# Kernel optimization log

Measured on AMD Instinct MI355X. Metric: run time of the kernel, lower is better.

## Reference

```python
import jax, jax.numpy as jnp
import numpy as np

N = 4096          # nodes (= Mamba sequence length)
E_EDGES = 65536   # edges
D = 512           # dim_h (= d_inner, expand=1)
NEXP = 4          # num_experts (cfg.model.num_experts)
DSTATE = 16
DCONV = 4
DTRANK = 32       # ceil(D/16)
EPS = 1e-5


def _silu(x):
    return x * jax.nn.sigmoid(x)


def _bn(h, g, b):
    # BatchNorm1d over node axis (batch statistics)
    mu = h.mean(0)
    var = h.var(0)
    return (h - mu) * jax.lax.rsqrt(var + EPS) * g + b


def _mamba(u, in_w, conv_w, conv_b, x_w, dt_w, dt_b, A_log, Dp, out_w):
    # u: [L, D] single-sequence Mamba(d_model=D, d_state=16, d_conv=4, expand=1)
    L = u.shape[0]
    xz = u @ in_w                      # [L, 2D]
    xc, z = xz[:, :D], xz[:, D:]
    xp = jnp.pad(xc, ((DCONV - 1, 0), (0, 0)))
    xconv = conv_b
    for k in range(DCONV):             # depthwise causal conv, tiny fixed loop
        xconv = xconv + conv_w[:, k] * xp[k:k + L]
    xs = _silu(xconv)                  # [L, D]
    dbc = xs @ x_w                     # [L, DTRANK + 2*DSTATE]
    dt = jax.nn.softplus(dbc[:, :DTRANK] @ dt_w + dt_b)          # [L, D]
    Bm = dbc[:, DTRANK:DTRANK + DSTATE]                          # [L, S]
    Cm = dbc[:, DTRANK + DSTATE:]                                # [L, S]
    A = -jnp.exp(A_log)                                          # [D, S]
    dA = jnp.exp(dt[:, :, None] * A[None])                       # [L, D, S]
    dBu = dt[:, :, None] * Bm[:, None, :] * xs[:, :, None]       # [L, D, S]

    def step(hprev, inp):
        dA_t, dBu_t, C_t = inp
        hn = dA_t * hprev + dBu_t
        return hn, (hn * C_t[None, :]).sum(-1)

    _, ys = jax.lax.scan(step, jnp.zeros((D, DSTATE), u.dtype), (dA, dBu, Cm))
    y = ys + Dp * xs
    return (y * _silu(z)) @ out_w      # [L, D]


def setup_inputs() -> dict:
    key = jax.random.key(0)
    ks = jax.random.split(key, 24)
    s = 1.0 / np.sqrt(D)
    inp = {}
    inp['x'] = jax.random.normal(ks[0], (N, D), jnp.float32)
    inp['edge_index'] = jax.random.randint(ks[1], (2, E_EDGES), 0, N)
    inp['edge_attr'] = jax.random.normal(ks[2], (E_EDGES, D), jnp.float32)
    # GINE nn: Linear(D,D) -> ReLU -> Linear(D,D)
    inp['gin_w1'] = jax.random.normal(ks[3], (D, D)) * s
    inp['gin_b1'] = jnp.zeros((D,))
    inp['gin_w2'] = jax.random.normal(ks[4], (D, D)) * s
    inp['gin_b2'] = jnp.zeros((D,))
    # BatchNorms
    inp['bn1l_g'] = jnp.ones((D,)); inp['bn1l_b'] = jnp.zeros((D,))
    inp['bn1a_g'] = jnp.ones((D,)); inp['bn1a_b'] = jnp.zeros((D,))
    inp['bn2_g'] = jnp.ones((D,)); inp['bn2_b'] = jnp.zeros((D,))
    # gating MLP [D, D//2, NEXP]
    inp['gate_w1'] = jax.random.normal(ks[5], (D, D // 2)) * s
    inp['gate_b1'] = jnp.zeros((D // 2,))
    inp['gate_w2'] = jax.random.normal(ks[6], (D // 2, NEXP)) * (1.0 / np.sqrt(D // 2))
    inp['gate_b2'] = jnp.zeros((NEXP,))
    # stacked per-expert Mamba params
    inp['in_w'] = jax.random.normal(ks[7], (NEXP, D, 2 * D)) * s
    inp['conv_w'] = jax.random.normal(ks[8], (NEXP, D, DCONV)) * 0.5
    inp['conv_b'] = jnp.zeros((NEXP, D))
    inp['x_w'] = jax.random.normal(ks[9], (NEXP, D, DTRANK + 2 * DSTATE)) * s
    inp['dt_w'] = jax.random.normal(ks[10], (NEXP, DTRANK, D)) * (1.0 / np.sqrt(DTRANK))
    inp['dt_b'] = jax.random.normal(ks[11], (NEXP, D)) * 0.1 - 4.0
    A0 = jnp.log(jnp.arange(1, DSTATE + 1, dtype=jnp.float32))
    inp['A_log'] = jnp.broadcast_to(A0, (NEXP, D, DSTATE)).copy()
    inp['Dp'] = jnp.ones((NEXP, D))
    inp['out_w'] = jax.random.normal(ks[12], (NEXP, D, D)) * s
    # FFN
    inp['ff_w1'] = jax.random.normal(ks[13], (D, 2 * D)) * s
    inp['ff_b1'] = jnp.zeros((2 * D,))
    inp['ff_w2'] = jax.random.normal(ks[14], (2 * D, D)) * (1.0 / np.sqrt(2 * D))
    inp['ff_b2'] = jnp.zeros((D,))
    return inp


def reference(x, edge_index, edge_attr,
              gin_w1, gin_b1, gin_w2, gin_b2,
              bn1l_g, bn1l_b, bn1a_g, bn1a_b, bn2_g, bn2_b,
              gate_w1, gate_b1, gate_w2, gate_b2,
              in_w, conv_w, conv_b, x_w, dt_w, dt_b, A_log, Dp, out_w,
              ff_w1, ff_b1, ff_w2, ff_b2):
    h_in = x
    src, dst = edge_index[0], edge_index[1]
    # local GINEConv: nn(x + sum_j relu(x_j + e_ji))
    msg = jax.nn.relu(x[src] + edge_attr)                      # [E, D]
    aggr = jax.ops.segment_sum(msg, dst, num_segments=N)       # [N, D]
    h_local = jax.nn.relu((x + aggr) @ gin_w1 + gin_b1) @ gin_w2 + gin_b2
    h_local = _bn(h_in + h_local, bn1l_g, bn1l_b)
    # gated mixture of Mamba experts
    gate = jax.nn.softmax(jax.nn.relu(x @ gate_w1 + gate_b1) @ gate_w2 + gate_b2, axis=-1)  # [N, NEXP]
    ys = jax.vmap(_mamba, in_axes=(None, 0, 0, 0, 0, 0, 0, 0, 0, 0))(
        x, in_w, conv_w, conv_b, x_w, dt_w, dt_b, A_log, Dp, out_w)  # [NEXP, N, D]
    h_attn = jnp.einsum('ne,end->nd', gate, ys)
    h_attn = _bn(h_in + h_attn, bn1a_g, bn1a_b)
    # fuse + FFN
    h = h_local + h_attn
    ff = jax.nn.relu(h @ ff_w1 + ff_b1) @ ff_w2 + ff_b2
    return _bn(h + ff, bn2_g, bn2_b)
```

## Files before the change

kernel.cpp:

```cpp
#include <hip/hip_runtime.h>
#include <hip/hip_bf16.h>
#include <math.h>

#define N_NODES 4096
#define E_EDGE 65536
#define D 512
#define NEXP 4
#define DSTATE 16
#define DCONV 4
#define DTRANK 32
#define EPS 1e-5f
#define LCHUNK 32
#define NCHUNK (N_NODES / LCHUNK)

typedef __hip_bfloat16 bf16;
typedef short bf16x8 __attribute__((ext_vector_type(8)));
typedef float f32x4 __attribute__((ext_vector_type(4)));
typedef unsigned short u16x4 __attribute__((ext_vector_type(4)));

__device__ __forceinline__ float siluf(float x) { return x / (1.f + __expf(-x)); }
__device__ __forceinline__ float softplusf(float x) {
  return (x > 20.f) ? x : log1pf(__expf(x));
}
__device__ __forceinline__ unsigned short f2bf(float v) {
  bf16 b = __float2bfloat16(v);
  return *reinterpret_cast<unsigned short*>(&b);
}

__device__ __forceinline__ void gload16(const void* g, void* l) {
  __builtin_amdgcn_global_load_lds(
      (const __attribute__((address_space(1))) void*)g,
      (__attribute__((address_space(3))) void*)l, 16, 0, 0);
}

template <int FN, int EPI>
__global__ __launch_bounds__(256, 2) void mm_k(
    const bf16* __restrict__ A, int lda, long sA,
    const bf16* __restrict__ Bt, int ldb, long sB,
    const float* __restrict__ bias,
    float* __restrict__ Cf, bf16* __restrict__ Cb, int ldc, long sC, int K) {
  constexpr int BN = FN * 32;
  __shared__ __align__(16) bf16 As[128 * 32];
  __shared__ __align__(16) bf16 Bs[BN * 32];
  const int z = blockIdx.z;
  A += (size_t)z * sA;
  Bt += (size_t)z * sB;
  const int tid = threadIdx.x;
  const int w = tid >> 6, l = tid & 63;
  const int wr = w >> 1, wc = w & 1;
  const int bm = blockIdx.y * 128, bn = blockIdx.x * BN;

  f32x4 acc[4][FN];
#pragma unroll
  for (int i = 0; i < 4; ++i)
#pragma unroll
    for (int j = 0; j < FN; ++j) acc[i][j] = 0.f;

  const int srow = l >> 2, schunk = l & 3;
  const bf16* gA = A + (size_t)(bm + w * 16 + srow) * lda + schunk * 8;
  const bf16* gB = Bt + (size_t)(bn + w * 16 + srow) * ldb + schunk * 8;
  bf16* lA = As + w * 512;
  bf16* lB = Bs + w * 512;

  const int ar = wr * 64 + (l & 15);
  const int br = wc * FN * 16 + (l & 15);
  const int kb = l >> 4;

  for (int k0 = 0; k0 < K; k0 += 32) {
    gload16(gA + k0, lA);
    gload16(gA + k0 + (size_t)64 * lda, lA + 64 * 32);
    gload16(gB + k0, lB);
    if (FN == 4) gload16(gB + k0 + (size_t)64 * ldb, lB + 64 * 32);
    __syncthreads();
    const bf16x8* Ap = (const bf16x8*)As;
    const bf16x8* Bp = (const bf16x8*)Bs;
    bf16x8 af[4], bfr[FN];
#pragma unroll
    for (int i = 0; i < 4; ++i) af[i] = Ap[(ar + i * 16) * 4 + kb];
#pragma unroll
    for (int j = 0; j < FN; ++j) bfr[j] = Bp[(br + j * 16) * 4 + kb];
#pragma unroll
    for (int i = 0; i < 4; ++i)
#pragma unroll
      for (int j = 0; j < FN; ++j)
        acc[i][j] = __builtin_amdgcn_mfma_f32_16x16x32_bf16(bfr[j], af[i], acc[i][j], 0, 0, 0);
    __syncthreads();
  }

  if (Cf) Cf += (size_t)z * sC;
  if (Cb) Cb += (size_t)z * sC;
  const int r0 = bm + wr * 64 + (l & 15);
  const int cb0 = bn + wc * FN * 16 + ((l >> 4) << 2);
#pragma unroll
  for (int i = 0; i < 4; ++i) {
    const int row = r0 + i * 16;
#pragma unroll
    for (int j = 0; j < FN; ++j) {
      const int col = cb0 + j * 16;
      f32x4 v = acc[i][j];
      if (bias) v += *(const f32x4*)&bias[col];
      if (EPI == 1) {
#pragma unroll
        for (int r = 0; r < 4; ++r) v[r] = fmaxf(v[r], 0.f);
      }
      if (Cf) *(f32x4*)&Cf[(size_t)row * ldc + col] = v;
      if (Cb) {
        u16x4 u;
#pragma unroll
        for (int r = 0; r < 4; ++r) u[r] = f2bf(v[r]);
        *(u16x4*)&Cb[(size_t)row * ldc + col] = u;
      }
    }
  }
}

struct WtArgs {
  const float* in[8];
  bf16* out[8];
  int K[8], N[8], ldo[8];
  long sin[8], sout[8];
  int cum[8];
};
__global__ __launch_bounds__(256) void wtrans_all_k(WtArgs a) {
  __shared__ float t[32][33];
  int b = blockIdx.x;
  int i = 0;
  while (b >= a.cum[i]) ++i;
  int local = b - (i ? a.cum[i - 1] : 0);
  const int ntx = a.N[i] / 32;
  const int nty = a.K[i] / 32;
  const int perz = ntx * nty;
  const int z = local / perz;
  const int rem = local - z * perz;
  const int bx = rem % ntx, by = rem / ntx;
  const float* in = a.in[i] + (size_t)z * a.sin[i];
  bf16* out = a.out[i] + (size_t)z * a.sout[i];
  const int N = a.N[i], ldo = a.ldo[i];
  const int n0 = bx * 32, k0 = by * 32;
  const int tx = threadIdx.x & 31, ty = threadIdx.x >> 5;
  for (int r = ty; r < 32; r += 8) t[r][tx] = in[(size_t)(k0 + r) * N + n0 + tx];
  __syncthreads();
  for (int r = ty; r < 32; r += 8)
    out[(size_t)(n0 + r) * ldo + k0 + tx] = __float2bfloat16(t[tx][r]);
}

__global__ void hist_k(const int* __restrict__ ei, int* __restrict__ deg) {
  int e = blockIdx.x * 256 + threadIdx.x;
  if (e < E_EDGE) atomicAdd(&deg[ei[E_EDGE + e]], 1);
}

__global__ __launch_bounds__(1024) void prefix_k(const int* __restrict__ deg,
                                                 int* __restrict__ rowstart) {
  __shared__ int s[1024];
  int t = threadIdx.x;
  int base = t * 4;
  int d0 = deg[base], d1 = deg[base + 1], d2 = deg[base + 2], d3 = deg[base + 3];
  int sum = d0 + d1 + d2 + d3;
  s[t] = sum;
  __syncthreads();
  for (int off = 1; off < 1024; off <<= 1) {
    int v = (t >= off) ? s[t - off] : 0;
    __syncthreads();
    s[t] += v;
    __syncthreads();
  }
  int excl = s[t] - sum;
  rowstart[base] = excl;
  rowstart[base + 1] = excl + d0;
  rowstart[base + 2] = excl + d0 + d1;
  rowstart[base + 3] = excl + d0 + d1 + d2;
}

__global__ void scatter_k(const int* __restrict__ ei, const int* __restrict__ rowstart,
                          int* __restrict__ cnt, int* __restrict__ eid) {
  int e = blockIdx.x * 256 + threadIdx.x;
  if (e < E_EDGE) {
    int dst = ei[E_EDGE + e];
    int slot = rowstart[dst] + atomicAdd(&cnt[dst], 1);
    eid[slot] = e;
  }
}

__global__ __launch_bounds__(256) void aggr_gather_k(
    const float* __restrict__ x, const int* __restrict__ ei, const float* __restrict__ ea,
    const int* __restrict__ rowstart, const int* __restrict__ deg,
    const int* __restrict__ eid, bf16* __restrict__ hpre, bf16* __restrict__ xbf) {
  int n = blockIdx.x;
  int tid = threadIdx.x;
  int beg = rowstart[n];
  int end = beg + deg[n];
  float a0 = 0.f, a1 = 0.f;
  int i = beg;
  for (; i + 1 < end; i += 2) {
    int e0 = eid[i], e1 = eid[i + 1];
    int s0 = ei[e0], s1 = ei[e1];
    const float* x0 = x + (size_t)s0 * D;
    const float* e0p = ea + (size_t)e0 * D;
    const float* x1 = x + (size_t)s1 * D;
    const float* e1p = ea + (size_t)e1 * D;
    a0 += fmaxf(x0[tid] + e0p[tid], 0.f) + fmaxf(x1[tid] + e1p[tid], 0.f);
    a1 += fmaxf(x0[tid + 256] + e0p[tid + 256], 0.f) +
          fmaxf(x1[tid + 256] + e1p[tid + 256], 0.f);
  }
  if (i < end) {
    int e0 = eid[i];
    int s0 = ei[e0];
    const float* x0 = x + (size_t)s0 * D;
    const float* e0p = ea + (size_t)e0 * D;
    a0 += fmaxf(x0[tid] + e0p[tid], 0.f);
    a1 += fmaxf(x0[tid + 256] + e0p[tid + 256], 0.f);
  }
  float xv0 = x[(size_t)n * D + tid];
  float xv1 = x[(size_t)n * D + tid + 256];
  hpre[(size_t)n * D + tid] = __float2bfloat16(xv0 + a0);
  hpre[(size_t)n * D + tid + 256] = __float2bfloat16(xv1 + a1);
  xbf[(size_t)n * D + tid] = __float2bfloat16(xv0);
  xbf[(size_t)n * D + tid + 256] = __float2bfloat16(xv1);
}

__global__ __launch_bounds__(256) void gate2_k(const float* __restrict__ g1,
                                               const float* __restrict__ w2,
                                               const float* __restrict__ b2,
                                               float* __restrict__ gate) {
  int row = blockIdx.x * 4 + (threadIdx.x >> 6);
  int lane = threadIdx.x & 63;
  float a0 = 0.f, a1 = 0.f, a2 = 0.f, a3 = 0.f;
  for (int k = lane; k < 256; k += 64) {
    float v = g1[(size_t)row * 256 + k];
    a0 = fmaf(v, w2[k * 4 + 0], a0);
    a1 = fmaf(v, w2[k * 4 + 1], a1);
    a2 = fmaf(v, w2[k * 4 + 2], a2);
    a3 = fmaf(v, w2[k * 4 + 3], a3);
  }
#pragma unroll
  for (int off = 32; off; off >>= 1) {
    a0 += __shfl_down(a0, off);
    a1 += __shfl_down(a1, off);
    a2 += __shfl_down(a2, off);
    a3 += __shfl_down(a3, off);
  }
  if (lane == 0) {
    float l0 = a0 + b2[0], l1 = a1 + b2[1], l2 = a2 + b2[2], l3 = a3 + b2[3];
    float m = fmaxf(fmaxf(l0, l1), fmaxf(l2, l3));
    float e0 = __expf(l0 - m), e1 = __expf(l1 - m), e2 = __expf(l2 - m), e3 = __expf(l3 - m);
    float s = 1.f / (e0 + e1 + e2 + e3);
    gate[row * 4 + 0] = e0 * s;
    gate[row * 4 + 1] = e1 * s;
    gate[row * 4 + 2] = e2 * s;
    gate[row * 4 + 3] = e3 * s;
  }
}

__global__ void conv_silu_k(const bf16* __restrict__ xz, const float* __restrict__ cw,
                            const float* __restrict__ cb, bf16* __restrict__ xs, int e0) {
  const int z = blockIdx.y;
  xz += (size_t)z * N_NODES * 2 * D;
  xs += (size_t)z * N_NODES * D;
  cw += (size_t)(e0 + z) * D * DCONV;
  cb += (size_t)(e0 + z) * D;
  int idx = blockIdx.x * blockDim.x + threadIdx.x;
  if (idx >= N_NODES * D) return;
  int t = idx >> 9;
  int d = idx & (D - 1);
  float acc = cb[d];
#pragma unroll
  for (int k = 0; k < DCONV; ++k) {
    int tt = t + k - (DCONV - 1);
    if (tt >= 0)
      acc = fmaf(cw[d * DCONV + k], __bfloat162float(xz[(size_t)tt * (2 * D) + d]), acc);
  }
  xs[idx] = __float2bfloat16(siluf(acc));
}

__global__ void dt_k(const float* __restrict__ dbc, const float* __restrict__ dtw,
                     const float* __restrict__ dtbias, bf16* __restrict__ dt, int e0) {
  const int z = blockIdx.y;
  dbc += (size_t)z * N_NODES * 64;
  dt += (size_t)z * N_NODES * D;
  dtw += (size_t)(e0 + z) * DTRANK * D;
  dtbias += (size_t)(e0 + z) * D;
  int idx = blockIdx.x * blockDim.x + threadIdx.x;
  int t = idx >> 9, d = idx & (D - 1);
  float acc = dtbias[d];
#pragma unroll
  for (int k = 0; k < DTRANK; ++k) acc = fmaf(dbc[t * 64 + k], dtw[k * D + d], acc);
  dt[idx] = __float2bfloat16(softplusf(acc));
}

__global__ __launch_bounds__(256) void colstats_k(const float* __restrict__ p,
                                                  const float* __restrict__ q,
                                                  float* __restrict__ acc) {
  __shared__ float sb[4][512], sb2[4][512];
  const int w = threadIdx.x >> 6, l = threadIdx.x & 63;
  float s[8], s2[8];
#pragma unroll
  for (int i = 0; i < 8; ++i) { s[i] = 0.f; s2[i] = 0.f; }
  for (int j = 0; j < 16; ++j) {
    size_t base = ((size_t)blockIdx.x * 64 + w * 16 + j) * D;
#pragma unroll
    for (int i = 0; i < 8; ++i) {
      int c = i * 64 + l;
      float v = p[base + c] + q[base + c];
      s[i] += v;
      s2[i] = fmaf(v, v, s2[i]);
    }
  }
#pragma unroll
  for (int i = 0; i < 8; ++i) {
    sb[w][i * 64 + l] = s[i];
    sb2[w][i * 64 + l] = s2[i];
  }
  __syncthreads();
  for (int c = threadIdx.x; c < 512; c += 256) {
    atomicAdd(&acc[c], sb[0][c] + sb[1][c] + sb[2][c] + sb[3][c]);
    atomicAdd(&acc[512 + c], sb2[0][c] + sb2[1][c] + sb2[2][c] + sb2[3][c]);
  }
}

__global__ __launch_bounds__(256) void colstats2_k(const float* __restrict__ x,
                                                   const float* __restrict__ p,
                                                   const float* __restrict__ q,
                                                   float* __restrict__ acc1,
                                                   float* __restrict__ acc2) {
  __shared__ float sb[4][512], sb2[4][512];
  const int w = threadIdx.x >> 6, l = threadIdx.x & 63;
  float s1[8], s1q[8], s2[8], s2q[8];
#pragma unroll
  for (int i = 0; i < 8; ++i) { s1[i] = 0.f; s1q[i] = 0.f; s2[i] = 0.f; s2q[i] = 0.f; }
  for (int j = 0; j < 16; ++j) {
    size_t base = ((size_t)blockIdx.x * 64 + w * 16 + j) * D;
#pragma unroll
    for (int i = 0; i < 8; ++i) {
      int c = i * 64 + l;
      float xv = x[base + c];
      float v1 = xv + p[base + c];
      float v2 = xv + q[base + c];
      s1[i] += v1;
      s1q[i] = fmaf(v1, v1, s1q[i]);
      s2[i] += v2;
      s2q[i] = fmaf(v2, v2, s2q[i]);
    }
  }
#pragma unroll
  for (int i = 0; i < 8; ++i) {
    sb[w][i * 64 + l] = s1[i];
    sb2[w][i * 64 + l] = s1q[i];
  }
  __syncthreads();
  for (int c = threadIdx.x; c < 512; c += 256) {
    atomicAdd(&acc1[c], sb[0][c] + sb[1][c] + sb[2][c] + sb[3][c]);
    atomicAdd(&acc1[512 + c], sb2[0][c] + sb2[1][c] + sb2[2][c] + sb2[3][c]);
  }
  __syncthreads();
#pragma unroll
  for (int i = 0; i < 8; ++i) {
    sb[w][i * 64 + l] = s2[i];
    sb2[w][i * 64 + l] = s2q[i];
  }
  __syncthreads();
  for (int c = threadIdx.x; c < 512; c += 256) {
    atomicAdd(&acc2[c], sb[0][c] + sb[1][c] + sb[2][c] + sb[3][c]);
    atomicAdd(&acc2[512 + c], sb2[0][c] + sb2[1][c] + sb2[2][c] + sb2[3][c]);
  }
}

__device__ __forceinline__ void bn_params(const float* acc, int d, float& mu, float& rsig) {
  mu = acc[d] * (1.f / N_NODES);
  float var = acc[512 + d] * (1.f / N_NODES) - mu * mu;
  rsig = rsqrtf(var + EPS);
}

__global__ void norm_k(const float* __restrict__ p, const float* __restrict__ q,
                       const float* __restrict__ acc, const float* __restrict__ g,
                       const float* __restrict__ b, float* __restrict__ o) {
  int idx = blockIdx.x * blockDim.x + threadIdx.x;
  if (idx >= N_NODES * D) return;
  int d = idx & (D - 1);
  float mu, rsig;
  bn_params(acc, d, mu, rsig);
  o[idx] = (p[idx] + q[idx] - mu) * rsig * g[d] + b[d];
}

__global__ void bnadd2_k(const float* __restrict__ x, const float* __restrict__ hloc,
                         const float* __restrict__ hattn, const float* __restrict__ acc1,
                         const float* __restrict__ acc2, const float* __restrict__ g1,
                         const float* __restrict__ b1, const float* __restrict__ g2,
                         const float* __restrict__ b2, float* __restrict__ of,
                         bf16* __restrict__ ob) {
  int idx = blockIdx.x * blockDim.x + threadIdx.x;
  if (idx >= N_NODES * D) return;
  int d = idx & (D - 1);
  float mu1, rs1, mu2, rs2;
  bn_params(acc1, d, mu1, rs1);
  bn_params(acc2, d, mu2, rs2);
  float xv = x[idx];
  float v = (xv + hloc[idx] - mu1) * rs1 * g1[d] + b1[d] +
            (xv + hattn[idx] - mu2) * rs2 * g2[d] + b2[d];
  of[idx] = v;
  ob[idx] = __float2bfloat16(v);
}

__global__ __launch_bounds__(512) void scanA_k(const bf16* __restrict__ dt,
                                               const bf16* __restrict__ xs,
                                               const float* __restrict__ dbc,
                                               const float* __restrict__ Alog,
                                               float* __restrict__ Q,
                                               float* __restrict__ dtsum, int e0) {
  const int z = blockIdx.y;
  dt += (size_t)z * N_NODES * D;
  xs += (size_t)z * N_NODES * D;
  dbc += (size_t)z * N_NODES * 64;
  Alog += (size_t)(e0 + z) * D * DSTATE;
  Q += (size_t)z * NCHUNK * D * DSTATE;
  dtsum += (size_t)z * NCHUNK * D;
  int c = blockIdx.x;
  int d = threadIdx.x;
  float As[DSTATE], h[DSTATE];
#pragma unroll
  for (int s = 0; s < DSTATE; ++s) {
    As[s] = -__expf(Alog[d * DSTATE + s]);
    h[s] = 0.f;
  }
  float dts = 0.f;
  int t0 = c * LCHUNK;
  for (int t = t0; t < t0 + LCHUNK; ++t) {
    float dtv = __bfloat162float(dt[(size_t)t * D + d]);
    float xv = __bfloat162float(xs[(size_t)t * D + d]);
    float bx = dtv * xv;
    dts += dtv;
#pragma unroll
    for (int s = 0; s < DSTATE; ++s) {
      float Bv = dbc[(size_t)t * 64 + DTRANK + s];
      h[s] = fmaf(__expf(dtv * As[s]), h[s], bx * Bv);
    }
  }
  size_t base = ((size_t)c * D + d) * DSTATE;
#pragma unroll
  for (int s = 0; s < DSTATE; ++s) Q[base + s] = h[s];
  dtsum[c * D + d] = dts;
}

__global__ __launch_bounds__(256) void scanB_k(const float* __restrict__ Q,
                                               const float* __restrict__ dtsum,
                                               const float* __restrict__ Alog,
                                               float* __restrict__ Hin, int e0) {
  const int z = blockIdx.y;
  Q += (size_t)z * NCHUNK * D * DSTATE;
  dtsum += (size_t)z * NCHUNK * D;
  Alog += (size_t)(e0 + z) * D * DSTATE;
  Hin += (size_t)z * NCHUNK * D * DSTATE;
  int idx = blockIdx.x * blockDim.x + threadIdx.x;
  int d = idx >> 4;
  float As = -__expf(Alog[idx]);
  float h = 0.f;
  for (int c = 0; c < NCHUNK; ++c) {
    size_t base = (size_t)c * D * DSTATE + idx;
    Hin[base] = h;
    h = fmaf(__expf(As * dtsum[c * D + d]), h, Q[base]);
  }
}

__global__ __launch_bounds__(512) void scanC_k(const bf16* __restrict__ dt,
                                               const bf16* __restrict__ xs,
                                               const float* __restrict__ dbc,
                                               const float* __restrict__ Alog,
                                               const float* __restrict__ Hin,
                                               const bf16* __restrict__ xz,
                                               const float* __restrict__ Dp,
                                               const float* __restrict__ gate,
                                               bf16* __restrict__ u, int e0) {
  const int z = blockIdx.y;
  dt += (size_t)z * N_NODES * D;
  xs += (size_t)z * N_NODES * D;
  dbc += (size_t)z * N_NODES * 64;
  Alog += (size_t)(e0 + z) * D * DSTATE;
  Hin += (size_t)z * NCHUNK * D * DSTATE;
  xz += (size_t)z * N_NODES * 2 * D;
  Dp += (size_t)(e0 + z) * D;
  u += (size_t)(e0 + z) * 512;
  const int ge = e0 + z;
  int c = blockIdx.x;
  int d = threadIdx.x;
  float As[DSTATE], h[DSTATE];
  size_t base = ((size_t)c * D + d) * DSTATE;
#pragma unroll
  for (int s = 0; s < DSTATE; ++s) {
    As[s] = -__expf(Alog[d * DSTATE + s]);
    h[s] = Hin[base + s];
  }
  float Dv = Dp[d];
  int t0 = c * LCHUNK;
  for (int t = t0; t < t0 + LCHUNK; ++t) {
    float dtv = __bfloat162float(dt[(size_t)t * D + d]);
    float xv = __bfloat162float(xs[(size_t)t * D + d]);
    float bx = dtv * xv;
    float y = 0.f;
#pragma unroll
    for (int s = 0; s < DSTATE; ++s) {
      float Bv = dbc[(size_t)t * 64 + DTRANK + s];
      float Cv = dbc[(size_t)t * 64 + DTRANK + DSTATE + s];
      h[s] = fmaf(__expf(dtv * As[s]), h[s], bx * Bv);
      y = fmaf(h[s], Cv, y);
    }
    float zv = __bfloat162float(xz[(size_t)t * (2 * D) + D + d]);
    float gv = gate[t * NEXP + ge];
    u[(size_t)t * 2048 + d] = __float2bfloat16(gv * (y + Dv * xv) * siluf(zv));
  }
}

extern "C" void kernel_launch(void* const* d_in, const int* in_sizes, int n_in,
                              void* d_out, int out_size, void* d_ws, size_t ws_size,
                              hipStream_t stream) {
  const float* x = (const float*)d_in[0];
  const int* ei = (const int*)d_in[1];
  const float* ea = (const float*)d_in[2];
  const float* gin_w1 = (const float*)d_in[3];
  const float* gin_b1 = (const float*)d_in[4];
  const float* gin_w2 = (const float*)d_in[5];
  const float* gin_b2 = (const float*)d_in[6];
  const float* bn1l_g = (const float*)d_in[7];
  const float* bn1l_b = (const float*)d_in[8];
  const float* bn1a_g = (const float*)d_in[9];
  const float* bn1a_b = (const float*)d_in[10];
  const float* bn2_g = (const float*)d_in[11];
  const float* bn2_b = (const float*)d_in[12];
  const float* gate_w1 = (const float*)d_in[13];
  const float* gate_b1 = (const float*)d_in[14];
  const float* gate_w2 = (const float*)d_in[15];
  const float* gate_b2 = (const float*)d_in[16];
  const float* in_w = (const float*)d_in[17];
  const float* conv_w = (const float*)d_in[18];
  const float* conv_b = (const float*)d_in[19];
  const float* x_w = (const float*)d_in[20];
  const float* dt_w = (const float*)d_in[21];
  const float* dt_b = (const float*)d_in[22];
  const float* A_log = (const float*)d_in[23];
  const float* Dp = (const float*)d_in[24];
  const float* out_w = (const float*)d_in[25];
  const float* ff_w1 = (const float*)d_in[26];
  const float* ff_b1 = (const float*)d_in[27];
  const float* ff_w2 = (const float*)d_in[28];
  const float* ff_b2 = (const float*)d_in[29];
  float* out = (float*)d_out;

  const size_t ND = (size_t)N_NODES * D;
  const size_t NDb = ND / 2;

  const size_t fixed_f = 3 * ND + (size_t)N_NODES * 256 + 16384 + 2490624 + ND + 2048 +
                         81920 + 2 * ND + 4096;
  const size_t per_f = 2 * ND + NDb + (size_t)N_NODES * 64 + NDb +
                       2 * (size_t)NCHUNK * D * DSTATE + (size_t)NCHUNK * D;
  const int EB = (ws_size >= (fixed_f + 4 * per_f + 65536) * sizeof(float)) ? 4 : 1;

  float* ws = (float*)d_ws;
  size_t off = 0;
  auto alloc = [&](size_t n) {
    float* p = ws + off;
    off += (n + 63) & ~(size_t)63;
    return p;
  };
  float* ffo = alloc(ND);
  float* pbuf = alloc(ND);
  float* hlocal = alloc(ND);
  float* g1 = alloc((size_t)N_NODES * 256);
  float* gate = alloc((size_t)N_NODES * NEXP);
  bf16* gw1t = (bf16*)alloc(131072);
  bf16* gw2t = (bf16*)alloc(131072);
  bf16* gatew1t = (bf16*)alloc(65536);
  bf16* inwt = (bf16*)alloc(1048576);
  bf16* xwt = (bf16*)alloc(65536);
  bf16* outwt_cat = (bf16*)alloc(524288);
  bf16* ffw1t = (bf16*)alloc(262144);
  bf16* ffw2t = (bf16*)alloc(262144);
  int* deg = (int*)alloc(N_NODES);
  int* cnt = (int*)alloc(N_NODES);
  float* accs = alloc(3072);
  int* eid = (int*)alloc(E_EDGE);
  int* rowstart = (int*)alloc(N_NODES);
  float* xbf_f = alloc(NDb);
  float* xz_f = alloc((size_t)EB * ND);
  float* xs_f = alloc((size_t)EB * NDb);
  float* dbc = alloc((size_t)EB * N_NODES * 64);
  float* dtb_f = alloc((size_t)EB * NDb);
  float* Qb = alloc((size_t)EB * NCHUNK * D * DSTATE);
  float* Hin = alloc((size_t)EB * NCHUNK * D * DSTATE);
  float* dtsum = alloc((size_t)EB * NCHUNK * D);
  float* ucat_f = alloc(4 * NDb);
  float* hattn_raw = alloc(ND);
  float* acc1 = accs, *acc2 = accs + 1024, *acc3 = accs + 2048;

  bf16* x_bf = (bf16*)xbf_f;
  bf16* hpre_bf = (bf16*)pbuf;
  bf16* t1_bf = (bf16*)(pbuf + NDb);
  bf16* xz_bf = (bf16*)xz_f;
  bf16* xs_bf = (bf16*)xs_f;
  bf16* dt_bf = (bf16*)dtb_f;
  bf16* ucat = (bf16*)ucat_f;
  float* hcomb = xz_f;
  bf16* hcomb_bf = (bf16*)(ucat_f);
  bf16* ffh_bf = (bf16*)pbuf;

  const int nelem = N_NODES * D;
  const int ew = (nelem + 255) / 256;

  hipMemsetAsync(deg, 0, (N_NODES + N_NODES + 3072) * sizeof(float), stream);

  WtArgs wa;
  const float* wsrc[8] = {gin_w1, gin_w2, gate_w1, in_w, x_w, out_w, ff_w1, ff_w2};
  bf16* wdst[8] = {gw1t, gw2t, gatew1t, inwt, xwt, outwt_cat, ffw1t, ffw2t};
  int wK[8] = {512, 512, 512, 512, 512, 512, 512, 1024};
  int wN[8] = {512, 512, 256, 1024, 64, 512, 1024, 512};
  int wldo[8] = {512, 512, 512, 512, 512, 2048, 512, 1024};
  long wsin[8] = {0, 0, 0, (long)512 * 1024, (long)512 * 64, (long)512 * 512, 0, 0};
  long wsout[8] = {0, 0, 0, (long)512 * 1024, (long)64 * 512, 512, 0, 0};
  int wz[8] = {1, 1, 1, 4, 4, 4, 1, 1};
  int cum = 0;
  for (int i = 0; i < 8; ++i) {
    wa.in[i] = wsrc[i];
    wa.out[i] = wdst[i];
    wa.K[i] = wK[i];
    wa.N[i] = wN[i];
    wa.ldo[i] = wldo[i];
    wa.sin[i] = wsin[i];
    wa.sout[i] = wsout[i];
    cum += (wN[i] / 32) * (wK[i] / 32) * wz[i];
    wa.cum[i] = cum;
  }
  wtrans_all_k<<<cum, 256, 0, stream>>>(wa);

  hist_k<<<E_EDGE / 256, 256, 0, stream>>>(ei, deg);
  prefix_k<<<1, 1024, 0, stream>>>(deg, rowstart);
  scatter_k<<<E_EDGE / 256, 256, 0, stream>>>(ei, rowstart, cnt, eid);
  aggr_gather_k<<<N_NODES, 256, 0, stream>>>(x, ei, ea, rowstart, deg, eid, hpre_bf, x_bf);
  mm_k<2, 1><<<dim3(8, 32, 1), 256, 0, stream>>>(hpre_bf, 512, 0, gw1t, 512, 0, gin_b1,
                                                 nullptr, t1_bf, 512, 0, 512);
  mm_k<2, 0><<<dim3(8, 32, 1), 256, 0, stream>>>(t1_bf, 512, 0, gw2t, 512, 0, gin_b2,
                                                 hlocal, nullptr, 512, 0, 512);

  mm_k<2, 1><<<dim3(4, 32, 1), 256, 0, stream>>>(x_bf, 512, 0, gatew1t, 512, 0, gate_b1,
                                                 g1, nullptr, 256, 0, 512);
  gate2_k<<<N_NODES / 4, 256, 0, stream>>>(g1, gate_w2, gate_b2, gate);

  for (int e0 = 0; e0 < NEXP; e0 += EB) {
    mm_k<4, 0><<<dim3(8, 32, EB), 256, 0, stream>>>(
        x_bf, 512, 0, inwt + (size_t)e0 * 512 * 1024, 512, (long)512 * 1024, nullptr,
        nullptr, xz_bf, 1024, (long)N_NODES * 1024, 512);
    conv_silu_k<<<dim3(ew, EB), 256, 0, stream>>>(xz_bf, conv_w, conv_b, xs_bf, e0);
    mm_k<2, 0><<<dim3(1, 32, EB), 256, 0, stream>>>(
        xs_bf, 512, (long)ND, xwt + (size_t)e0 * 64 * 512, 512, (long)64 * 512, nullptr,
        dbc, nullptr, 64, (long)N_NODES * 64, 512);
    dt_k<<<dim3(ew, EB), 256, 0, stream>>>(dbc, dt_w, dt_b, dt_bf, e0);
    scanA_k<<<dim3(NCHUNK, EB), 512, 0, stream>>>(dt_bf, xs_bf, dbc, A_log, Qb, dtsum, e0);
    scanB_k<<<dim3((D * DSTATE) / 256, EB), 256, 0, stream>>>(Qb, dtsum, A_log, Hin, e0);
    scanC_k<<<dim3(NCHUNK, EB), 512, 0, stream>>>(dt_bf, xs_bf, dbc, A_log, Hin, xz_bf, Dp,
                                                  gate, ucat, e0);
  }
  mm_k<2, 0><<<dim3(8, 32, 1), 256, 0, stream>>>(ucat, 2048, 0, outwt_cat, 2048, 0,
                                                 nullptr, hattn_raw, nullptr, 512, 0, 2048);

  colstats2_k<<<64, 256, 0, stream>>>(x, hlocal, hattn_raw, acc1, acc2);
  bnadd2_k<<<ew, 256, 0, stream>>>(x, hlocal, hattn_raw, acc1, acc2, bn1l_g, bn1l_b,
                                   bn1a_g, bn1a_b, hcomb, hcomb_bf);
  mm_k<4, 1><<<dim3(8, 32, 1), 256, 0, stream>>>(hcomb_bf, 512, 0, ffw1t, 512, 0, ff_b1,
                                                 nullptr, ffh_bf, 1024, 0, 512);
  mm_k<2, 0><<<dim3(8, 32, 1), 256, 0, stream>>>(ffh_bf, 1024, 0, ffw2t, 1024, 0, ff_b2,
                                                 ffo, nullptr, 512, 0, 1024);
  colstats_k<<<64, 256, 0, stream>>>(hcomb, ffo, acc3);
  norm_k<<<ew, 256, 0, stream>>>(hcomb, ffo, acc3, bn2_g, bn2_b, out);
}
```

Baseline: 460.0 us.

## Double-buffer GEMM LDS tiles and fuse BatchNorm column stats into GEMM epilogue

Adds double-buffered shared-memory staging to the bf16 MFMA GEMM, so the next K tile is loaded while the current one is computed and one barrier per iteration is dropped. Adds a STATS epilogue that adds a residual tensor, reduces per-column sum and sum-of-squares across lanes, and atomically accumulates them. This removes the separate colstats kernels and their extra full passes over the activations. In exchange LDS use doubles, which may limit occupancy, and there are more atomics per output tile.

```diff
diff --git a/kernel.cpp b/kernel.cpp
--- a/kernel.cpp
+++ b/kernel.cpp
@@ -33,15 +33,16 @@
       (__attribute__((address_space(3))) void*)l, 16, 0, 0);
 }
 
-template <int FN, int EPI>
+template <int FN, int EPI, bool STATS>
 __global__ __launch_bounds__(256, 2) void mm_k(
     const bf16* __restrict__ A, int lda, long sA,
     const bf16* __restrict__ Bt, int ldb, long sB,
     const float* __restrict__ bias,
-    float* __restrict__ Cf, bf16* __restrict__ Cb, int ldc, long sC, int K) {
+    float* __restrict__ Cf, bf16* __restrict__ Cb, int ldc, long sC, int K,
+    const float* __restrict__ part, float* __restrict__ sacc) {
   constexpr int BN = FN * 32;
-  __shared__ __align__(16) bf16 As[128 * 32];
-  __shared__ __align__(16) bf16 Bs[BN * 32];
+  __shared__ __align__(16) bf16 As[2][128 * 32];
+  __shared__ __align__(16) bf16 Bs[2][BN * 32];
   const int z = blockIdx.z;
   A += (size_t)z * sA;
   Bt += (size_t)z * sB;
@@ -59,21 +60,25 @@
   const int srow = l >> 2, schunk = l & 3;
   const bf16* gA = A + (size_t)(bm + w * 16 + srow) * lda + schunk * 8;
   const bf16* gB = Bt + (size_t)(bn + w * 16 + srow) * ldb + schunk * 8;
-  bf16* lA = As + w * 512;
-  bf16* lB = Bs + w * 512;
 
   const int ar = wr * 64 + (l & 15);
   const int br = wc * FN * 16 + (l & 15);
   const int kb = l >> 4;
 
+  auto stage = [&](int b, int k0) {
+    gload16(gA + k0, As[b] + w * 512);
+    gload16(gA + k0 + (size_t)64 * lda, As[b] + 64 * 32 + w * 512);
+    gload16(gB + k0, Bs[b] + w * 512);
+    if (FN == 4) gload16(gB + k0 + (size_t)64 * ldb, Bs[b] + 64 * 32 + w * 512);
+  };
+
+  stage(0, 0);
+  __syncthreads();
+  int cur = 0;
   for (int k0 = 0; k0 < K; k0 += 32) {
-    gload16(gA + k0, lA);
-    gload16(gA + k0 + (size_t)64 * lda, lA + 64 * 32);
-    gload16(gB + k0, lB);
-    if (FN == 4) gload16(gB + k0 + (size_t)64 * ldb, lB + 64 * 32);
-    __syncthreads();
-    const bf16x8* Ap = (const bf16x8*)As;
-    const bf16x8* Bp = (const bf16x8*)Bs;
+    if (k0 + 32 < K) stage(cur ^ 1, k0 + 32);
+    const bf16x8* Ap = (const bf16x8*)As[cur];
+    const bf16x8* Bp = (const bf16x8*)Bs[cur];
     bf16x8 af[4], bfr[FN];
 #pragma unroll
     for (int i = 0; i < 4; ++i) af[i] = Ap[(ar + i * 16) * 4 + kb];
@@ -85,12 +90,18 @@
       for (int j = 0; j < FN; ++j)
         acc[i][j] = __builtin_amdgcn_mfma_f32_16x16x32_bf16(bfr[j], af[i], acc[i][j], 0, 0, 0);
     __syncthreads();
+    cur ^= 1;
   }
 
   if (Cf) Cf += (size_t)z * sC;
   if (Cb) Cb += (size_t)z * sC;
   const int r0 = bm + wr * 64 + (l & 15);
   const int cb0 = bn + wc * FN * 16 + ((l >> 4) << 2);
+  f32x4 ssum[FN], ssq[FN];
+  if (STATS) {
+#pragma unroll
+    for (int j = 0; j < FN; ++j) { ssum[j] = 0.f; ssq[j] = 0.f; }
+  }
 #pragma unroll
   for (int i = 0; i < 4; ++i) {
     const int row = r0 + i * 16;
@@ -110,6 +121,33 @@
         for (int r = 0; r < 4; ++r) u[r] = f2bf(v[r]);
         *(u16x4*)&Cb[(size_t)row * ldc + col] = u;
       }
+      if (STATS) {
+        f32x4 p = *(const f32x4*)&part[(size_t)row * ldc + col];
+        f32x4 t = v + p;
+        ssum[j] += t;
+        ssq[j] += t * t;
+      }
+    }
+  }
+  if (STATS) {
+#pragma unroll
+    for (int m = 1; m < 16; m <<= 1) {
+#pragma unroll
+      for (int j = 0; j < FN; ++j)
+#pragma unroll
+        for (int r = 0; r < 4; ++r) {
+          ssum[j][r] += __shfl_xor(ssum[j][r], m);
+          ssq[j][r] += __shfl_xor(ssq[j][r], m);
+        }
+    }
+    if ((l & 15) == 0) {
+#pragma unroll
+      for (int j = 0; j < FN; ++j)
+#pragma unroll
+        for (int r = 0; r < 4; ++r) {
+          atomicAdd(&sacc[cb0 + j * 16 + r], ssum[j][r]);
+          atomicAdd(&sacc[512 + cb0 + j * 16 + r], ssq[j][r]);
+        }
     }
   }
 }
@@ -285,83 +323,6 @@
 #pragma unroll
   for (int k = 0; k < DTRANK; ++k) acc = fmaf(dbc[t * 64 + k], dtw[k * D + d], acc);
   dt[idx] = __float2bfloat16(softplusf(acc));
-}
-
-__global__ __launch_bounds__(256) void colstats_k(const float* __restrict__ p,
-                                                  const float* __restrict__ q,
-                                                  float* __restrict__ acc) {
-  __shared__ float sb[4][512], sb2[4][512];
-  const int w = threadIdx.x >> 6, l = threadIdx.x & 63;
-  float s[8], s2[8];
-#pragma unroll
-  for (int i = 0; i < 8; ++i) { s[i] = 0.f; s2[i] = 0.f; }
-  for (int j = 0; j < 16; ++j) {
-    size_t base = ((size_t)blockIdx.x * 64 + w * 16 + j) * D;
-#pragma unroll
-    for (int i = 0; i < 8; ++i) {
-      int c = i * 64 + l;
-      float v = p[base + c] + q[base + c];
-      s[i] += v;
-      s2[i] = fmaf(v, v, s2[i]);
-    }
-  }
-#pragma unroll
-  for (int i = 0; i < 8; ++i) {
-    sb[w][i * 64 + l] = s[i];
-    sb2[w][i * 64 + l] = s2[i];
-  }
-  __syncthreads();
-  for (int c = threadIdx.x; c < 512; c += 256) {
-    atomicAdd(&acc[c], sb[0][c] + sb[1][c] + sb[2][c] + sb[3][c]);
-    atomicAdd(&acc[512 + c], sb2[0][c] + sb2[1][c] + sb2[2][c] + sb2[3][c]);
-  }
-}
-
-__global__ __launch_bounds__(256) void colstats2_k(const float* __restrict__ x,
-                                                   const float* __restrict__ p,
-                                                   const float* __restrict__ q,
-                                                   float* __restrict__ acc1,
-                                                   float* __restrict__ acc2) {
-  __shared__ float sb[4][512], sb2[4][512];
-  const int w = threadIdx.x >> 6, l = threadIdx.x & 63;
-  float s1[8], s1q[8], s2[8], s2q[8];
-#pragma unroll
-  for (int i = 0; i < 8; ++i) { s1[i] = 0.f; s1q[i] = 0.f; s2[i] = 0.f; s2q[i] = 0.f; }
-  for (int j = 0; j < 16; ++j) {
-    size_t base = ((size_t)blockIdx.x * 64 + w * 16 + j) * D;
-#pragma unroll
-    for (int i = 0; i < 8; ++i) {
-      int c = i * 64 + l;
-      float xv = x[base + c];
-      float v1 = xv + p[base + c];
-      float v2 = xv + q[base + c];
-      s1[i] += v1;
-      s1q[i] = fmaf(v1, v1, s1q[i]);
-      s2[i] += v2;
-      s2q[i] = fmaf(v2, v2, s2q[i]);
-    }
-  }
-#pragma unroll
-  for (int i = 0; i < 8; ++i) {
-    sb[w][i * 64 + l] = s1[i];
-    sb2[w][i * 64 + l] = s1q[i];
-  }
-  __syncthreads();
-  for (int c = threadIdx.x; c < 512; c += 256) {
-    atomicAdd(&acc1[c], sb[0][c] + sb[1][c] + sb[2][c] + sb[3][c]);
-    atomicAdd(&acc1[512 + c], sb2[0][c] + sb2[1][c] + sb2[2][c] + sb2[3][c]);
-  }
-  __syncthreads();
-#pragma unroll
-  for (int i = 0; i < 8; ++i) {
-    sb[w][i * 64 + l] = s2[i];
-    sb2[w][i * 64 + l] = s2q[i];
-  }
-  __syncthreads();
-  for (int c = threadIdx.x; c < 512; c += 256) {
-    atomicAdd(&acc2[c], sb[0][c] + sb[1][c] + sb[2][c] + sb[3][c]);
-    atomicAdd(&acc2[512 + c], sb2[0][c] + sb2[1][c] + sb2[2][c] + sb2[3][c]);
-  }
 }
 
 __device__ __forceinline__ void bn_params(const float* acc, int d, float& mu, float& rsig) {
@@ -632,39 +593,40 @@
   prefix_k<<<1, 1024, 0, stream>>>(deg, rowstart);
   scatter_k<<<E_EDGE / 256, 256, 0, stream>>>(ei, rowstart, cnt, eid);
   aggr_gather_k<<<N_NODES, 256, 0, stream>>>(x, ei, ea, rowstart, deg, eid, hpre_bf, x_bf);
-  mm_k<2, 1><<<dim3(8, 32, 1), 256, 0, stream>>>(hpre_bf, 512, 0, gw1t, 512, 0, gin_b1,
-                                                 nullptr, t1_bf, 512, 0, 512);
-  mm_k<2, 0><<<dim3(8, 32, 1), 256, 0, stream>>>(t1_bf, 512, 0, gw2t, 512, 0, gin_b2,
-                                                 hlocal, nullptr, 512, 0, 512);
-
-  mm_k<2, 1><<<dim3(4, 32, 1), 256, 0, stream>>>(x_bf, 512, 0, gatew1t, 512, 0, gate_b1,
-                                                 g1, nullptr, 256, 0, 512);
+  mm_k<2, 1, false><<<dim3(8, 32, 1), 256, 0, stream>>>(
+      hpre_bf, 512, 0, gw1t, 512, 0, gin_b1, nullptr, t1_bf, 512, 0, 512, nullptr,
+      nullptr);
+  mm_k<2, 0, true><<<dim3(8, 32, 1), 256, 0, stream>>>(
+      t1_bf, 512, 0, gw2t, 512, 0, gin_b2, hlocal, nullptr, 512, 0, 512, x, acc1);
+
+  mm_k<2, 1, false><<<dim3(4, 32, 1), 256, 0, stream>>>(
+      x_bf, 512, 0, gatew1t, 512, 0, gate_b1, g1, nullptr, 256, 0, 512, nullptr, nullptr);
   gate2_k<<<N_NODES / 4, 256, 0, stream>>>(g1, gate_w2, gate_b2, gate);
 
   for (int e0 = 0; e0 < NEXP; e0 += EB) {
-    mm_k<4, 0><<<dim3(8, 32, EB), 256, 0, stream>>>(
+    mm_k<4, 0, false><<<dim3(8, 32, EB), 256, 0, stream>>>(
         x_bf, 512, 0, inwt + (size_t)e0 * 512 * 1024, 512, (long)512 * 1024, nullptr,
-        nullptr, xz_bf, 1024, (long)N_NODES * 1024, 512);
+        nullptr, xz_bf, 1024, (long)N_NODES * 1024, 512, nullptr, nullptr);
     conv_silu_k<<<dim3(ew, EB), 256, 0, stream>>>(xz_bf, conv_w, conv_b, xs_bf, e0);
-    mm_k<2, 0><<<dim3(1, 32, EB), 256, 0, stream>>>(
+    mm_k<2, 0, false><<<dim3(1, 32, EB), 256, 0, stream>>>(
         xs_bf, 512, (long)ND, xwt + (size_t)e0 * 64 * 512, 512, (long)64 * 512, nullptr,
-        dbc, nullptr, 64, (long)N_NODES * 64, 512);
+        dbc, nullptr, 64, (long)N_NODES * 64, 512, nullptr, nullptr);
     dt_k<<<dim3(ew, EB), 256, 0, stream>>>(dbc, dt_w, dt_b, dt_bf, e0);
     scanA_k<<<dim3(NCHUNK, EB), 512, 0, stream>>>(dt_bf, xs_bf, dbc, A_log, Qb, dtsum, e0);
     scanB_k<<<dim3((D * DSTATE) / 256, EB), 256, 0, stream>>>(Qb, dtsum, A_log, Hin, e0);
     scanC_k<<<dim3(NCHUNK, EB), 512, 0, stream>>>(dt_bf, xs_bf, dbc, A_log, Hin, xz_bf, Dp,
                                                   gate, ucat, e0);
   }
-  mm_k<2, 0><<<dim3(8, 32, 1), 256, 0, stream>>>(ucat, 2048, 0, outwt_cat, 2048, 0,
-                                                 nullptr, hattn_raw, nullptr, 512, 0, 2048);
-
-  colstats2_k<<<64, 256, 0, stream>>>(x, hlocal, hattn_raw, acc1, acc2);
+  mm_k<2, 0, true><<<dim3(8, 32, 1), 256, 0, stream>>>(
+      ucat, 2048, 0, outwt_cat, 2048, 0, nullptr, hattn_raw, nullptr, 512, 0, 2048, x,
+      acc2);
+
   bnadd2_k<<<ew, 256, 0, stream>>>(x, hlocal, hattn_raw, acc1, acc2, bn1l_g, bn1l_b,
                                    bn1a_g, bn1a_b, hcomb, hcomb_bf);
-  mm_k<4, 1><<<dim3(8, 32, 1), 256, 0, stream>>>(hcomb_bf, 512, 0, ffw1t, 512, 0, ff_b1,
-                                                 nullptr, ffh_bf, 1024, 0, 512);
-  mm_k<2, 0><<<dim3(8, 32, 1), 256, 0, stream>>>(ffh_bf, 1024, 0, ffw2t, 1024, 0, ff_b2,
-                                                 ffo, nullptr, 512, 0, 1024);
-  colstats_k<<<64, 256, 0, stream>>>(hcomb, ffo, acc3);
+  mm_k<4, 1, false><<<dim3(8, 32, 1), 256, 0, stream>>>(
+      hcomb_bf, 512, 0, ffw1t, 512, 0, ff_b1, nullptr, ffh_bf, 1024, 0, 512, nullptr,
+      nullptr);
+  mm_k<2, 0, true><<<dim3(8, 32, 1), 256, 0, stream>>>(
+      ffh_bf, 1024, 0, ffw2t, 1024, 0, ff_b2, ffo, nullptr, 512, 0, 1024, hcomb, acc3);
   norm_k<<<ew, 256, 0, stream>>>(hcomb, ffo, acc3, bn2_g, bn2_b, out);
 }
```

Result: no change. 464.6 us (+1.0%).
